# Optimization experiments

Measured on AMD Instinct MI355X. Metric: run time of the kernel, lower is better.

Reference implementation:

```python
import jax, jax.numpy as jnp
import numpy as np
import math

CHUNK = 64

def _linear(x, W, b):
    # torch nn.Linear: y = x @ W.T + b
    return jnp.einsum('bsd,ed->bse', x, W) + b

def setup_inputs() -> dict:
    key = jax.random.key(0)
    ks = jax.random.split(key, 10)
    B, S, D = 4, 4096, 512
    scale = 0.02
    inp = {
        'x': jax.random.normal(ks[0], (B, S, D), jnp.float32),
        'base_phases': jax.random.normal(ks[1], (S, D), jnp.float32) * math.pi,
        'Wk': jax.random.normal(ks[2], (D, D), jnp.float32) * scale,
        'bk': jnp.zeros((D,), jnp.float32),
        'Wv': jax.random.normal(ks[3], (D, D), jnp.float32) * scale,
        'bv': jnp.zeros((D,), jnp.float32),
        'Wq': jax.random.normal(ks[4], (D, D), jnp.float32) * scale,
        'bq': jnp.zeros((D,), jnp.float32),
        'Wkm': jax.random.normal(ks[5], (D, D), jnp.float32) * scale,
        'bkm': jnp.zeros((D,), jnp.float32),
        'Wqm': jax.random.normal(ks[6], (D, D), jnp.float32) * scale,
        'bqm': jnp.zeros((D,), jnp.float32),
        'mod_scale': jnp.ones((1,), jnp.float32) * 0.1,
        'ln_g': jnp.ones((D,), jnp.float32),
        'ln_b': jnp.zeros((D,), jnp.float32),
        'Wo': jax.random.normal(ks[7], (D, D), jnp.float32) * scale,
        'bo': jnp.zeros((D,), jnp.float32),
    }
    return inp

def reference(x, base_phases, Wk, bk, Wv, bv, Wq, bq, Wkm, bkm, Wqm, bqm, mod_scale, ln_g, ln_b, Wo, bo):
    B, S, D = x.shape
    bp = base_phases[:S][None]                      # [1,S,D]
    key = _linear(x, Wk, bk)
    value = _linear(x, Wv, bv)
    query = _linear(x, Wq, bq)
    key_phase = bp + _linear(key, Wkm, bkm) * mod_scale
    query_phase = bp + _linear(query, Wqm, bqm) * mod_scale
    bound_real = value * jnp.cos(key_phase)
    bound_imag = value * jnp.sin(key_phase)
    # chunked cumulative memory (S divisible by CHUNK -> no padding)
    nC = S // CHUNK
    br = bound_real.reshape(B, nC, CHUNK, D)
    bi = bound_imag.reshape(B, nC, CHUNK, D)
    qp = query_phase.reshape(B, nC, CHUNK, D)
    mem_real = jnp.cumsum(br, axis=2)
    mem_imag = jnp.cumsum(bi, axis=2)
    retrieved = (mem_real * jnp.cos(qp) + mem_imag * jnp.sin(qp)).reshape(B, S, D)
    retrieved = retrieved / math.sqrt(D)
    # LayerNorm + Linear (to_out)
    mu = jnp.mean(retrieved, axis=-1, keepdims=True)
    var = jnp.mean((retrieved - mu) ** 2, axis=-1, keepdims=True)
    normed = (retrieved - mu) / jnp.sqrt(var + 1e-5) * ln_g + ln_b
    out = _linear(normed, Wo, bo)
    return x + out
```

## Files before the change

### kernel.cpp

```cpp
#include <hip/hip_runtime.h>
#include <hip/hip_bf16.h>


typedef __attribute__((ext_vector_type(8))) short short8;
typedef __attribute__((ext_vector_type(4))) float f32x4;

#define M_TOK   16384
#define DIM     512
#define SEQ     4096
#define NCHUNK  64

__device__ __forceinline__ void gll16(const void* g, void* l) {
  __builtin_amdgcn_global_load_lds(
      (const __attribute__((address_space(1))) unsigned int*)g,
      (__attribute__((address_space(3))) unsigned int*)l, 16, 0, 0);
}

__global__ __launch_bounds__(256) void cvt_f32_bf16(
    const float* __restrict__ s, __hip_bfloat16* __restrict__ d, int n4) {
  int i = blockIdx.x * 256 + threadIdx.x;
  if (i >= n4) return;
  float4 v = ((const float4*)s)[i];
  union { __hip_bfloat16 h[4]; uint2 u; } t;
  t.h[0] = __float2bfloat16(v.x);
  t.h[1] = __float2bfloat16(v.y);
  t.h[2] = __float2bfloat16(v.z);
  t.h[3] = __float2bfloat16(v.w);
  ((uint2*)d)[i] = t.u;
}

__global__ __launch_bounds__(256) void pack_weights(
    const float* __restrict__ wk, const float* __restrict__ wv,
    const float* __restrict__ wq, const float* __restrict__ wkm,
    const float* __restrict__ wqm, const float* __restrict__ wo,
    const float* __restrict__ bk, const float* __restrict__ bv,
    const float* __restrict__ bq,
    __hip_bfloat16* __restrict__ Wall, float* __restrict__ bc1) {
  int t = blockIdx.x * 256 + threadIdx.x;
  int m = t >> 16;
  int r = (t & 65535) * 4;
  const float* src;
  switch (m) {
    case 0: src = wk;  break;
    case 1: src = wv;  break;
    case 2: src = wq;  break;
    case 3: src = wkm; break;
    case 4: src = wqm; break;
    default: src = wo; break;
  }
  float4 v = *(const float4*)(src + r);
  union { __hip_bfloat16 h[4]; uint2 u; } o;
  o.h[0] = __float2bfloat16(v.x);
  o.h[1] = __float2bfloat16(v.y);
  o.h[2] = __float2bfloat16(v.z);
  o.h[3] = __float2bfloat16(v.w);
  ((uint2*)(Wall + (size_t)m * 262144))[r >> 2] = o.u;
  if (t < 1536) {
    float b = (t < 512) ? bk[t] : (t < 1024) ? bv[t - 512] : bq[t - 1024];
    bc1[t] = b;
  }
}

template <int EPI>
__global__ __launch_bounds__(256) void gemm_bt(
    const __hip_bfloat16* __restrict__ A, int lda,
    const __hip_bfloat16* __restrict__ Bt,
    const float* __restrict__ bias,
    void* __restrict__ Cout, int ldc,
    const float* __restrict__ resid) {
  constexpr int K = 512, BK = 32;
  __shared__ __align__(16) __hip_bfloat16 As[128 * BK];
  __shared__ __align__(16) __hip_bfloat16 Bs[128 * BK];

  const int tid  = threadIdx.x;
  const int lane = tid & 63;
  const int w    = tid >> 6;
  const int wm   = w >> 1;
  const int wn   = w & 1;
  const int m0   = blockIdx.y * 128;
  const int n0   = blockIdx.x * 128;

  const int rS0    = (w * 2 + 0) * 16 + (lane >> 2);
  const int rS1    = (w * 2 + 1) * 16 + (lane >> 2);
  const int kInRow = (lane & 3) * 8;
  const __hip_bfloat16* gA0 = A + (size_t)(m0 + rS0) * lda + kInRow;
  const __hip_bfloat16* gA1 = A + (size_t)(m0 + rS1) * lda + kInRow;
  const __hip_bfloat16* gB0 = Bt + (size_t)(n0 + rS0) * K + kInRow;
  const __hip_bfloat16* gB1 = Bt + (size_t)(n0 + rS1) * K + kInRow;
  char* ldsA0 = (char*)As + (w * 2 + 0) * 1024;
  char* ldsA1 = (char*)As + (w * 2 + 1) * 1024;
  char* ldsB0 = (char*)Bs + (w * 2 + 0) * 1024;
  char* ldsB1 = (char*)Bs + (w * 2 + 1) * 1024;

  f32x4 acc[4][4] = {};

  const int rfA = lane & 15;
  const int rfK = (lane >> 4) * 8;

  for (int kt = 0; kt < K; kt += BK) {
    __syncthreads();
    gll16(gA0 + kt, ldsA0);
    gll16(gA1 + kt, ldsA1);
    gll16(gB0 + kt, ldsB0);
    gll16(gB1 + kt, ldsB1);
    __syncthreads();

    short8 af[4], bf[4];
#pragma unroll
    for (int i = 0; i < 4; i++)
      af[i] = *(const short8*)(As + (wm * 64 + i * 16 + rfA) * BK + rfK);
#pragma unroll
    for (int j = 0; j < 4; j++)
      bf[j] = *(const short8*)(Bs + (wn * 64 + j * 16 + rfA) * BK + rfK);
#pragma unroll
    for (int i = 0; i < 4; i++)
#pragma unroll
      for (int j = 0; j < 4; j++)
        acc[i][j] = __builtin_amdgcn_mfma_f32_16x16x32_bf16(
            af[i], bf[j], acc[i][j], 0, 0, 0);
  }

  const int cq = lane >> 4;
#pragma unroll
  for (int i = 0; i < 4; i++) {
    int row = m0 + wm * 64 + i * 16 + cq * 4;
#pragma unroll
    for (int j = 0; j < 4; j++) {
      int col = n0 + wn * 64 + j * 16 + (lane & 15);
      float bz = bias[col];
#pragma unroll
      for (int r = 0; r < 4; r++) {
        float v = acc[i][j][r] + bz;
        size_t o = (size_t)(row + r) * ldc + col;
        if (EPI == 0) {
          ((__hip_bfloat16*)Cout)[o] = __float2bfloat16(v);
        } else {
          ((float*)Cout)[o] = v + resid[o];
        }
      }
    }
  }
}

__global__ __launch_bounds__(512) void phase_cumsum_ln(
    const __hip_bfloat16* __restrict__ KVQ,
    const __hip_bfloat16* __restrict__ Kmod,
    const __hip_bfloat16* __restrict__ Qmod,
    const float* __restrict__ bp,
    const float* __restrict__ mod_scale,
    const float* __restrict__ ln_g, const float* __restrict__ ln_b,
    __hip_bfloat16* __restrict__ normed) {
  __shared__ __hip_bfloat16 R[64 * 512];
  const int d      = threadIdx.x;
  const int blk    = blockIdx.x;
  const int token0 = blk * 64;
  const int sg0    = (blk & (NCHUNK - 1)) * 64;
  const float msc  = mod_scale[0];
  const float inv_sqrt_d = 0.044194173824159216f;

  float mr = 0.f, mi = 0.f;
  for (int s = 0; s < 64; ++s) {
    size_t t = (size_t)(token0 + s);
    float v  = __bfloat162float(KVQ[t * 1536 + 512 + d]);
    float km = __bfloat162float(Kmod[t * 512 + d]);
    float qm = __bfloat162float(Qmod[t * 512 + d]);
    float b  = bp[(size_t)(sg0 + s) * 512 + d];
    float kp = b + km * msc;
    float qp = b + qm * msc;
    float sk, ck, sq, cq;
    __sincosf(kp, &sk, &ck);
    __sincosf(qp, &sq, &cq);
    mr += v * ck;
    mi += v * sk;
    R[s * 512 + d] = __float2bfloat16((mr * cq + mi * sq) * inv_sqrt_d);
  }
  __syncthreads();

  const int lane = threadIdx.x & 63;
  const int wv   = threadIdx.x >> 6;
  float gj[8], bj[8];
#pragma unroll
  for (int j = 0; j < 8; j++) {
    int col = lane + 64 * j;
    gj[j] = ln_g[col];
    bj[j] = ln_b[col];
  }
  for (int rr = 0; rr < 8; ++rr) {
    int row = wv * 8 + rr;
    float vals[8], sum = 0.f, sq2 = 0.f;
#pragma unroll
    for (int j = 0; j < 8; j++) {
      float x = __bfloat162float(R[row * 512 + lane + 64 * j]);
      vals[j] = x;
      sum += x;
      sq2 += x * x;
    }
#pragma unroll
    for (int off = 32; off; off >>= 1) {
      sum += __shfl_xor(sum, off, 64);
      sq2 += __shfl_xor(sq2, off, 64);
    }
    float mu   = sum * (1.f / 512.f);
    float var  = sq2 * (1.f / 512.f) - mu * mu;
    float rstd = rsqrtf(var + 1e-5f);
    size_t base = (size_t)(token0 + row) * 512;
#pragma unroll
    for (int j = 0; j < 8; j++) {
      int col = lane + 64 * j;
      float nv = (vals[j] - mu) * rstd * gj[j] + bj[j];
      normed[base + col] = __float2bfloat16(nv);
    }
  }
}

extern "C" void kernel_launch(void* const* d_in, const int* in_sizes, int n_in,
                              void* d_out, int out_size, void* d_ws,
                              size_t ws_size, hipStream_t stream) {
  const float* x    = (const float*)d_in[0];
  const float* bp   = (const float*)d_in[1];
  const float* Wk   = (const float*)d_in[2];
  const float* bk   = (const float*)d_in[3];
  const float* Wv   = (const float*)d_in[4];
  const float* bv   = (const float*)d_in[5];
  const float* Wq   = (const float*)d_in[6];
  const float* bq   = (const float*)d_in[7];
  const float* Wkm  = (const float*)d_in[8];
  const float* bkm  = (const float*)d_in[9];
  const float* Wqm  = (const float*)d_in[10];
  const float* bqm  = (const float*)d_in[11];
  const float* msc  = (const float*)d_in[12];
  const float* lng  = (const float*)d_in[13];
  const float* lnb  = (const float*)d_in[14];
  const float* Wo   = (const float*)d_in[15];
  const float* bo   = (const float*)d_in[16];
  float* out = (float*)d_out;

  char* ws = (char*)d_ws;
  __hip_bfloat16* x_bf = (__hip_bfloat16*)ws;  ws += (size_t)M_TOK * DIM * 2;
  __hip_bfloat16* Wall = (__hip_bfloat16*)ws;  ws += (size_t)6 * 262144 * 2;
  float*          bc1  = (float*)ws;           ws += 1536 * 4;
  __hip_bfloat16* KVQ  = (__hip_bfloat16*)ws;  ws += (size_t)M_TOK * 1536 * 2;
  __hip_bfloat16* Kmod = (__hip_bfloat16*)ws;  ws += (size_t)M_TOK * DIM * 2;
  __hip_bfloat16* Qmod = (__hip_bfloat16*)ws;  ws += (size_t)M_TOK * DIM * 2;
  __hip_bfloat16* nrm  = (__hip_bfloat16*)ws;  ws += (size_t)M_TOK * DIM * 2;

  cvt_f32_bf16<<<8192, 256, 0, stream>>>(x, x_bf, 2097152);
  pack_weights<<<1536, 256, 0, stream>>>(Wk, Wv, Wq, Wkm, Wqm, Wo, bk, bv, bq,
                                         Wall, bc1);
  gemm_bt<0><<<dim3(12, 128), 256, 0, stream>>>(x_bf, DIM, Wall, bc1, KVQ,
                                                1536, nullptr);
  gemm_bt<0><<<dim3(4, 128), 256, 0, stream>>>(KVQ + 0, 1536,
                                               Wall + (size_t)3 * 262144, bkm,
                                               Kmod, DIM, nullptr);
  gemm_bt<0><<<dim3(4, 128), 256, 0, stream>>>(KVQ + 1024, 1536,
                                               Wall + (size_t)4 * 262144, bqm,
                                               Qmod, DIM, nullptr);
  phase_cumsum_ln<<<256, 512, 0, stream>>>(KVQ, Kmod, Qmod, bp, msc, lng, lnb,
                                           nrm);
  gemm_bt<1><<<dim3(4, 128), 256, 0, stream>>>(nrm, DIM,
                                               Wall + (size_t)5 * 262144, bo,
                                               out, DIM, x);
}
```

Before: 248.2 us.

## Fold modulation linears into composed weights to drop two chained GEMMs

Precomputes Wkm·Wk and Wqm·Wq (plus the composed biases) on device each call, so the first GEMM directly produces V, Kmod and Qmod in one 1536-wide output. This removes the two dependent 512x512 GEMMs over all tokens and their intermediate buffers, and the phase kernel now reads a single interleaved buffer. It adds a small fp32 weight-composition GEMM per call, and rounding the composed product to bf16 once slightly changes numerics compared with the two-step chain.

```diff
diff --git a/kernel.cpp b/kernel.cpp
--- a/kernel.cpp
+++ b/kernel.cpp
@@ -7,7 +7,6 @@
 
 #define M_TOK   16384
 #define DIM     512
-#define SEQ     4096
 #define NCHUNK  64
 
 __device__ __forceinline__ void gll16(const void* g, void* l) {
@@ -29,36 +28,78 @@
   ((uint2*)d)[i] = t.u;
 }
 
-__global__ __launch_bounds__(256) void pack_weights(
-    const float* __restrict__ wk, const float* __restrict__ wv,
-    const float* __restrict__ wq, const float* __restrict__ wkm,
-    const float* __restrict__ wqm, const float* __restrict__ wo,
-    const float* __restrict__ bk, const float* __restrict__ bv,
-    const float* __restrict__ bq,
-    __hip_bfloat16* __restrict__ Wall, float* __restrict__ bc1) {
+__global__ __launch_bounds__(256) void pack_w2(
+    const float* __restrict__ Wv, const float* __restrict__ Wo,
+    const float* __restrict__ bv, __hip_bfloat16* __restrict__ Wall,
+    float* __restrict__ bc1) {
   int t = blockIdx.x * 256 + threadIdx.x;
   int m = t >> 16;
   int r = (t & 65535) * 4;
-  const float* src;
-  switch (m) {
-    case 0: src = wk;  break;
-    case 1: src = wv;  break;
-    case 2: src = wq;  break;
-    case 3: src = wkm; break;
-    case 4: src = wqm; break;
-    default: src = wo; break;
-  }
+  const float* src = m ? Wo : Wv;
+  __hip_bfloat16* dst = Wall + (m ? (size_t)1536 * 512 : 0);
   float4 v = *(const float4*)(src + r);
   union { __hip_bfloat16 h[4]; uint2 u; } o;
   o.h[0] = __float2bfloat16(v.x);
   o.h[1] = __float2bfloat16(v.y);
   o.h[2] = __float2bfloat16(v.z);
   o.h[3] = __float2bfloat16(v.w);
-  ((uint2*)(Wall + (size_t)m * 262144))[r >> 2] = o.u;
-  if (t < 1536) {
-    float b = (t < 512) ? bk[t] : (t < 1024) ? bv[t - 512] : bq[t - 1024];
-    bc1[t] = b;
-  }
+  ((uint2*)dst)[r >> 2] = o.u;
+  if (t < 512) bc1[t] = bv[t];
+}
+
+__global__ __launch_bounds__(256) void compose_w(
+    const float* __restrict__ Wkm, const float* __restrict__ Wk,
+    const float* __restrict__ Wqm, const float* __restrict__ Wq,
+    __hip_bfloat16* __restrict__ Wall) {
+  const float* Am = blockIdx.z ? Wqm : Wkm;
+  const float* Bm = blockIdx.z ? Wq : Wk;
+  __hip_bfloat16* C = Wall + (size_t)(512 + blockIdx.z * 512) * 512;
+  __shared__ float As[32][33];
+  __shared__ float Bs[32][33];
+  const int tid = threadIdx.x;
+  const int tx = tid & 31, ty = tid >> 5;
+  const int bi = blockIdx.y * 32, bj = blockIdx.x * 32;
+  float acc[4] = {0.f, 0.f, 0.f, 0.f};
+  for (int kt = 0; kt < 512; kt += 32) {
+#pragma unroll
+    for (int l = tid; l < 1024; l += 256) {
+      int r = l >> 5, c = l & 31;
+      As[r][c] = Am[(size_t)(bi + r) * 512 + kt + c];
+      Bs[r][c] = Bm[(size_t)(kt + r) * 512 + bj + c];
+    }
+    __syncthreads();
+#pragma unroll 8
+    for (int k = 0; k < 32; k++) {
+      float b = Bs[k][tx];
+#pragma unroll
+      for (int rr = 0; rr < 4; rr++) acc[rr] += As[ty + rr * 8][k] * b;
+    }
+    __syncthreads();
+  }
+#pragma unroll
+  for (int rr = 0; rr < 4; rr++)
+    C[(size_t)(bi + ty + rr * 8) * 512 + bj + tx] = __float2bfloat16(acc[rr]);
+}
+
+__global__ __launch_bounds__(512) void compose_b(
+    const float* __restrict__ Wkm, const float* __restrict__ bk,
+    const float* __restrict__ bkm, const float* __restrict__ Wqm,
+    const float* __restrict__ bq, const float* __restrict__ bqm,
+    float* __restrict__ bc1) {
+  const int z = blockIdx.x;
+  const int i = threadIdx.x;
+  const float* Wm = z ? Wqm : Wkm;
+  const float* b0 = z ? bq : bk;
+  const float* bm = z ? bqm : bkm;
+  float acc = bm[i];
+  const float4* w4 = (const float4*)(Wm + (size_t)i * 512);
+  const float4* b4 = (const float4*)b0;
+  for (int k = 0; k < 128; k++) {
+    float4 w = w4[k];
+    float4 bb = b4[k];
+    acc += w.x * bb.x + w.y * bb.y + w.z * bb.z + w.w * bb.w;
+  }
+  bc1[512 + z * 512 + i] = acc;
 }
 
 template <int EPI>
@@ -143,9 +184,7 @@
 }
 
 __global__ __launch_bounds__(512) void phase_cumsum_ln(
-    const __hip_bfloat16* __restrict__ KVQ,
-    const __hip_bfloat16* __restrict__ Kmod,
-    const __hip_bfloat16* __restrict__ Qmod,
+    const __hip_bfloat16* __restrict__ VKQ,
     const float* __restrict__ bp,
     const float* __restrict__ mod_scale,
     const float* __restrict__ ln_g, const float* __restrict__ ln_b,
@@ -161,9 +200,9 @@
   float mr = 0.f, mi = 0.f;
   for (int s = 0; s < 64; ++s) {
     size_t t = (size_t)(token0 + s);
-    float v  = __bfloat162float(KVQ[t * 1536 + 512 + d]);
-    float km = __bfloat162float(Kmod[t * 512 + d]);
-    float qm = __bfloat162float(Qmod[t * 512 + d]);
+    float v  = __bfloat162float(VKQ[t * 1536 + d]);
+    float km = __bfloat162float(VKQ[t * 1536 + 512 + d]);
+    float qm = __bfloat162float(VKQ[t * 1536 + 1024 + d]);
     float b  = bp[(size_t)(sg0 + s) * 512 + d];
     float kp = b + km * msc;
     float qp = b + qm * msc;
@@ -237,27 +276,19 @@
 
   char* ws = (char*)d_ws;
   __hip_bfloat16* x_bf = (__hip_bfloat16*)ws;  ws += (size_t)M_TOK * DIM * 2;
-  __hip_bfloat16* Wall = (__hip_bfloat16*)ws;  ws += (size_t)6 * 262144 * 2;
+  __hip_bfloat16* Wall = (__hip_bfloat16*)ws;  ws += (size_t)2048 * 512 * 2;
   float*          bc1  = (float*)ws;           ws += 1536 * 4;
-  __hip_bfloat16* KVQ  = (__hip_bfloat16*)ws;  ws += (size_t)M_TOK * 1536 * 2;
-  __hip_bfloat16* Kmod = (__hip_bfloat16*)ws;  ws += (size_t)M_TOK * DIM * 2;
-  __hip_bfloat16* Qmod = (__hip_bfloat16*)ws;  ws += (size_t)M_TOK * DIM * 2;
+  __hip_bfloat16* VKQ  = (__hip_bfloat16*)ws;  ws += (size_t)M_TOK * 1536 * 2;
   __hip_bfloat16* nrm  = (__hip_bfloat16*)ws;  ws += (size_t)M_TOK * DIM * 2;
 
   cvt_f32_bf16<<<8192, 256, 0, stream>>>(x, x_bf, 2097152);
-  pack_weights<<<1536, 256, 0, stream>>>(Wk, Wv, Wq, Wkm, Wqm, Wo, bk, bv, bq,
-                                         Wall, bc1);
-  gemm_bt<0><<<dim3(12, 128), 256, 0, stream>>>(x_bf, DIM, Wall, bc1, KVQ,
+  pack_w2<<<512, 256, 0, stream>>>(Wv, Wo, bv, Wall, bc1);
+  compose_w<<<dim3(16, 16, 2), 256, 0, stream>>>(Wkm, Wk, Wqm, Wq, Wall);
+  compose_b<<<2, 512, 0, stream>>>(Wkm, bk, bkm, Wqm, bq, bqm, bc1);
+  gemm_bt<0><<<dim3(12, 128), 256, 0, stream>>>(x_bf, DIM, Wall, bc1, VKQ,
                                                 1536, nullptr);
-  gemm_bt<0><<<dim3(4, 128), 256, 0, stream>>>(KVQ + 0, 1536,
-                                               Wall + (size_t)3 * 262144, bkm,
-                                               Kmod, DIM, nullptr);
-  gemm_bt<0><<<dim3(4, 128), 256, 0, stream>>>(KVQ + 1024, 1536,
-                                               Wall + (size_t)4 * 262144, bqm,
-                                               Qmod, DIM, nullptr);
-  phase_cumsum_ln<<<256, 512, 0, stream>>>(KVQ, Kmod, Qmod, bp, msc, lng, lnb,
-                                           nrm);
+  phase_cumsum_ln<<<256, 512, 0, stream>>>(VKQ, bp, msc, lng, lnb, nrm);
   gemm_bt<1><<<dim3(4, 128), 256, 0, stream>>>(nrm, DIM,
-                                               Wall + (size_t)5 * 262144, bo,
+                                               Wall + (size_t)1536 * 512, bo,
                                                out, DIM, x);
 }
```

Result: slower. 290.6 us (+17.1%).
